# Performance work log

Measured on AMD Instinct MI355X. Metric: run time of the kernel, lower is better.

The kernel has to match this reference:

```python
import jax, jax.numpy as jnp
import numpy as np

B, N, C = 8, 1024, 768
HEADS = 8
HD = C // HEADS  # head_dim = qk_dim // num_heads since qk_ratio=1
SCALE = HD ** (-0.5)


def setup_inputs() -> dict:
    key = jax.random.key(0)
    ks = jax.random.split(key, 8)
    s = 0.02
    return {
        "x": jax.random.normal(ks[0], (B, N, C), dtype=jnp.float32),
        "y": jax.random.normal(ks[1], (B, N, C), dtype=jnp.float32),
        "relative_pos": jax.random.normal(ks[2], (HEADS, N, N), dtype=jnp.float32),
        "H": 32,
        "W": 32,
        "Wq": jax.random.normal(ks[3], (C, C), dtype=jnp.float32) * s,
        "Wk": jax.random.normal(ks[4], (C, C), dtype=jnp.float32) * s,
        "Wv": jax.random.normal(ks[5], (C, C), dtype=jnp.float32) * s,
        "Wp": jax.random.normal(ks[6], (C, C), dtype=jnp.float32) * s,
        "bp": jnp.zeros((C,), dtype=jnp.float32),
    }


def reference(x, y, relative_pos, H, W, Wq, Wk, Wv, Wp, bp):
    # sr_ratio == 1 path: K/V come directly from y (no spatial reduction).
    b, n, c = x.shape
    q = (x @ Wq.T).reshape(b, n, HEADS, HD)       # bnhd
    k = (y @ Wk.T).reshape(b, n, HEADS, HD)       # bmhd
    v = (y @ Wv.T).reshape(b, n, HEADS, HD)       # bmhd
    # scores: QK^T * scale + learned relative position bias (broadcast over batch)
    attn = jnp.einsum("bnhd,bmhd->bhnm", q, k) * SCALE + relative_pos[None]
    attn = jax.nn.softmax(attn, axis=-1)
    out = jnp.einsum("bhnm,bmhd->bnhd", attn, v).reshape(b, n, c)
    return out @ Wp.T + bp
```

## Files before the change

kernel.cpp:

```cpp
#include <hip/hip_runtime.h>
#include <hip/hip_bf16.h>
#include <cstdint>
#include <cstddef>


using f32x4  = __attribute__((ext_vector_type(4))) float;
using bf16x8 = __attribute__((ext_vector_type(8))) __bf16;

constexpr int Bb = 8, Nn = 1024, Cc = 768;
constexpr float LOG2E = 1.4426950408889634f;
constexpr float QSC   = 0.10206207261596575f * 1.4426950408889634f;

__device__ __forceinline__ uint16_t f2bf(float f) {
  union { float f; uint32_t u; } v; v.f = f;
  return (uint16_t)((v.u + 0x7fffu + ((v.u >> 16) & 1u)) >> 16);
}

__device__ __forceinline__ void gl_lds16(const void* g, void* l) {
  __builtin_amdgcn_global_load_lds(
      (const __attribute__((address_space(1))) void*)g,
      (__attribute__((address_space(3))) void*)l, 16, 0, 0);
}

__device__ __forceinline__ f32x4 mfma16(bf16x8 a, bf16x8 b, f32x4 c) {
  return __builtin_amdgcn_mfma_f32_16x16x32_bf16(a, b, c, 0, 0, 0);
}

template <int CTRL>
__device__ __forceinline__ float dpp_add(float v) {
  union { float f; int i; } u, r;
  u.f = v;
  r.i = __builtin_amdgcn_update_dpp(u.i, u.i, CTRL, 0xF, 0xF, false);
  return v + r.f;
}
__device__ __forceinline__ float red16_add(float v) {
  v = dpp_add<0x128>(v);
  v = dpp_add<0x124>(v);
  v = dpp_add<0x122>(v);
  v = dpp_add<0x121>(v);
  return v;
}

__global__ void cvt2_kernel(const float* __restrict__ a,
                            const float* __restrict__ b,
                            uint16_t* __restrict__ da,
                            uint16_t* __restrict__ db, int n4) {
  int i = blockIdx.x * blockDim.x + threadIdx.x;
  const float* s = blockIdx.y ? b : a;
  uint16_t* d = blockIdx.y ? db : da;
  if (i < n4) {
    float4 v = ((const float4*)s)[i];
    ushort4 o;
    o.x = f2bf(v.x); o.y = f2bf(v.y); o.z = f2bf(v.z); o.w = f2bf(v.w);
    ((ushort4*)d)[i] = o;
  }
}

__global__ void cvtw_kernel(const float* __restrict__ wq,
                            const float* __restrict__ wk,
                            const float* __restrict__ wv,
                            const float* __restrict__ wp,
                            uint16_t* __restrict__ dq, uint16_t* __restrict__ dk,
                            uint16_t* __restrict__ dv, uint16_t* __restrict__ dp,
                            int n4) {
  int i = blockIdx.x * blockDim.x + threadIdx.x;
  const float* s; uint16_t* d; float sc = 1.f;
  switch (blockIdx.y) {
    case 0:  s = wq; d = dq; sc = QSC; break;
    case 1:  s = wk; d = dk; break;
    case 2:  s = wv; d = dv; break;
    default: s = wp; d = dp; break;
  }
  if (i < n4) {
    float4 v = ((const float4*)s)[i];
    ushort4 o;
    o.x = f2bf(v.x * sc); o.y = f2bf(v.y * sc);
    o.z = f2bf(v.z * sc); o.w = f2bf(v.w * sc);
    ((ushort4*)d)[i] = o;
  }
}

__device__ __forceinline__ void gemm_core(const uint16_t* __restrict__ A,
                                          const uint16_t* __restrict__ Bt,
                                          int m0, int n0, f32x4 (&acc)[4][4]) {
  __shared__ uint16_t As[128 * 64];
  __shared__ uint16_t Bs[128 * 64];
  const int tid = threadIdx.x;
  const int lane = tid & 63, l16 = lane & 15, quad = lane >> 4;
  const int w = tid >> 6;
  const int wm = (w & 1) * 64, wn = (w >> 1) * 64;

  int soff[4];
#pragma unroll
  for (int i = 0; i < 4; ++i) {
    int idx = tid + 256 * i;
    int row = idx >> 3, pc = idx & 7;
    int c = pc ^ (row & 7);
    soff[i] = row * 768 + c * 8;
  }

  for (int k0 = 0; k0 < 768; k0 += 64) {
    __syncthreads();
#pragma unroll
    for (int i = 0; i < 4; ++i)
      gl_lds16(A + (size_t)m0 * 768 + k0 + soff[i], &As[(tid + 256 * i) * 8]);
#pragma unroll
    for (int i = 0; i < 4; ++i)
      gl_lds16(Bt + (size_t)n0 * 768 + k0 + soff[i], &Bs[(tid + 256 * i) * 8]);
    __syncthreads();

#pragma unroll
    for (int ks = 0; ks < 2; ++ks) {
      bf16x8 a[4], b[4];
      const int phys = (ks * 4 + quad) ^ (l16 & 7);
#pragma unroll
      for (int i = 0; i < 4; ++i)
        a[i] = *(const bf16x8*)&As[(wm + i * 16 + l16) * 64 + phys * 8];
#pragma unroll
      for (int j = 0; j < 4; ++j)
        b[j] = *(const bf16x8*)&Bs[(wn + j * 16 + l16) * 64 + phys * 8];
#pragma unroll
      for (int i = 0; i < 4; ++i)
#pragma unroll
        for (int j = 0; j < 4; ++j)
          acc[i][j] = mfma16(a[i], b[j], acc[i][j]);
    }
  }
}

__global__ __launch_bounds__(256, 3) void qkv_kernel(
    const uint16_t* __restrict__ xb, const uint16_t* __restrict__ yb,
    const uint16_t* __restrict__ wq, const uint16_t* __restrict__ wk,
    const uint16_t* __restrict__ wv, uint16_t* __restrict__ Qb,
    uint16_t* __restrict__ Kb, uint16_t* __restrict__ Vt) {
  const int seg = blockIdx.x / 6, nb = blockIdx.x % 6;
  const uint16_t* A  = (seg == 0) ? xb : yb;
  const uint16_t* Bt = (seg == 0) ? wq : (seg == 1) ? wk : wv;
  const int m0 = blockIdx.y * 128, n0 = nb * 128;

  f32x4 acc[4][4] = {};
  gemm_core(A, Bt, m0, n0, acc);

  const int tid = threadIdx.x, lane = tid & 63;
  const int l16 = lane & 15, quad = lane >> 4, w = tid >> 6;
  const int wm = (w & 1) * 64, wn = (w >> 1) * 64;

  if (seg <= 1) {
    uint16_t* O = seg ? Kb : Qb;
#pragma unroll
    for (int i = 0; i < 4; ++i)
#pragma unroll
      for (int j = 0; j < 4; ++j) {
        int col = n0 + wn + j * 16 + l16;
#pragma unroll
        for (int r = 0; r < 4; ++r) {
          int row = m0 + wm + i * 16 + quad * 4 + r;
          O[(size_t)row * 768 + col] = f2bf(acc[i][j][r]);
        }
      }
  } else {
#pragma unroll
    for (int i = 0; i < 4; ++i) {
      int row0 = m0 + wm + i * 16 + quad * 4;
      int bidx = row0 >> 10, nseq = row0 & 1023;
#pragma unroll
      for (int j = 0; j < 4; ++j) {
        int col = n0 + wn + j * 16 + l16;
        int h = col / 96, hd = col % 96;
        ushort4 pk;
        pk.x = f2bf(acc[i][j][0]); pk.y = f2bf(acc[i][j][1]);
        pk.z = f2bf(acc[i][j][2]); pk.w = f2bf(acc[i][j][3]);
        size_t o = (((size_t)(bidx * 8 + h) * 96 + hd) << 10) + nseq;
        *(ushort4*)(Vt + o) = pk;
      }
    }
  }
}

__global__ __launch_bounds__(256, 3) void proj_kernel(
    const uint16_t* __restrict__ A, const uint16_t* __restrict__ Bt,
    float* __restrict__ out, const float* __restrict__ bias) {
  const int m0 = blockIdx.y * 128, n0 = blockIdx.x * 128;
  f32x4 acc[4][4] = {};
  gemm_core(A, Bt, m0, n0, acc);

  const int tid = threadIdx.x, lane = tid & 63;
  const int l16 = lane & 15, quad = lane >> 4, w = tid >> 6;
  const int wm = (w & 1) * 64, wn = (w >> 1) * 64;
  float bv[4];
#pragma unroll
  for (int j = 0; j < 4; ++j) bv[j] = bias[n0 + wn + j * 16 + l16];
#pragma unroll
  for (int i = 0; i < 4; ++i)
#pragma unroll
    for (int j = 0; j < 4; ++j) {
      int col = n0 + wn + j * 16 + l16;
#pragma unroll
      for (int r = 0; r < 4; ++r) {
        int row = m0 + wm + i * 16 + quad * 4 + r;
        out[(size_t)row * 768 + col] = acc[i][j][r] + bv[j];
      }
    }
}

__global__ __launch_bounds__(512, 4) void attn_kernel(
    const uint16_t* __restrict__ Q,
    const uint16_t* __restrict__ Kb,
    const uint16_t* __restrict__ Vt,
    const float* __restrict__ rel,
    uint16_t* __restrict__ AO) {
  __shared__ uint16_t Ks[2][64 * 96];
  __shared__ uint16_t Vs[2][96 * 64];
  __shared__ uint16_t Ps[128 * 64];

  const int tid = threadIdx.x;
  const int q0 = blockIdx.x * 128;
  const int bh = blockIdx.y;
  const int b = bh >> 3, h = bh & 7;
  const int w = tid >> 6, lane = tid & 63;
  const int l16 = lane & 15, quad = lane >> 4;
  const int l7 = l16 & 7;

  const int qrow = q0 + w * 16 + l16;
  bf16x8 qf[3];
  {
    const uint16_t* qp =
        Q + ((size_t)(b * 1024 + qrow)) * 768 + h * 96 + quad * 8;
#pragma unroll
    for (int j = 0; j < 3; ++j) qf[j] = *(const bf16x8*)(qp + j * 32);
  }

  auto kSrc = [](int c) {
    int r = c / 12, pc = c % 12;
    int kc = (pc < 8) ? (pc ^ (r & 7)) : (8 + ((pc & 3) ^ (r & 3)));
    return r * 768 + kc * 8;
  };
  auto vSrc = [](int c) {
    int d = c >> 3, pc = c & 7;
    return d * 1024 + (pc ^ (d & 7)) * 8;
  };
  const int  kc0 = tid;
  const int  ks0 = kSrc(kc0);
  const bool isK1 = (tid < 256);
  const int  c1 = isK1 ? (512 + tid) : (tid - 256);
  const int  s1 = isK1 ? kSrc(c1) : vSrc(c1);
  const int  vc2 = 256 + tid;
  const int  vs2 = vSrc(vc2);

  const uint16_t* kslab = Kb + ((size_t)(b * 1024)) * 768 + h * 96;
  const uint16_t* vslab = Vt + ((size_t)(bh * 96) << 10);
  const float* relbase =
      rel + ((size_t)h << 20) + ((size_t)(q0 + w * 16 + quad * 4) << 10) + l16;

  auto stage = [&](int knext, int bufi) {
    const uint16_t* kb = kslab + (size_t)knext * 768;
    const uint16_t* vb = vslab + knext;
    uint16_t* Kbuf = &Ks[bufi][0];
    uint16_t* Vbuf = &Vs[bufi][0];
    gl_lds16(kb + ks0, Kbuf + kc0 * 8);
    if (isK1) gl_lds16(kb + s1, Kbuf + c1 * 8);
    else      gl_lds16(vb + s1, Vbuf + c1 * 8);
    gl_lds16(vb + vs2, Vbuf + vc2 * 8);
  };

  float relv[2][16];
  auto loadrel = [&](int knext, float (&dst)[16]) {
#pragma unroll
    for (int r = 0; r < 4; ++r)
#pragma unroll
      for (int nt = 0; nt < 4; ++nt)
        dst[nt * 4 + r] = relbase[(size_t)r * 1024 + knext + nt * 16];
  };

  float l_i[4] = {0.f, 0.f, 0.f, 0.f};
  f32x4 o_acc[6] = {};

  stage(0, 0);
  loadrel(0, relv[0]);

#pragma unroll 2
  for (int kt = 0; kt < 16; ++kt) {
    const int cur = kt & 1, nxt = (kt + 1) & 1;
    __syncthreads();
    if (kt < 15) {
      stage((kt + 1) * 64, nxt);
      loadrel((kt + 1) * 64, relv[nxt]);
    }
    const uint16_t* KsC = &Ks[cur][0];
    const uint16_t* VsC = &Vs[cur][0];
    const float* rv = relv[cur];

    f32x4 s[4] = {};
#pragma unroll
    for (int ksi = 0; ksi < 3; ++ksi) {
#pragma unroll
      for (int nt = 0; nt < 4; ++nt) {
        const int row = nt * 16 + l16;
        const int c = ksi * 4 + quad;
        const int phys =
            (ksi < 2) ? (c ^ (row & 7)) : (8 + ((c & 3) ^ (row & 3)));
        bf16x8 kf = *(const bf16x8*)&KsC[row * 96 + phys * 8];
        s[nt] = mfma16(qf[ksi], kf, s[nt]);
      }
    }

    float pv[16];
#pragma unroll
    for (int nt = 0; nt < 4; ++nt)
#pragma unroll
      for (int r = 0; r < 4; ++r)
        pv[nt * 4 + r] =
            __builtin_amdgcn_exp2f(fmaf(rv[nt * 4 + r], LOG2E, s[nt][r]));
#pragma unroll
    for (int r = 0; r < 4; ++r)
      l_i[r] += (pv[r] + pv[4 + r]) + (pv[8 + r] + pv[12 + r]);

    const int khi = l16 >> 3;
#pragma unroll
    for (int r = 0; r < 4; ++r) {
      const int qloc = quad * 4 + r;
      const int rowoff = (w * 16 + qloc) * 64;
      const int sw = qloc & 7;
#pragma unroll
      for (int nt = 0; nt < 4; ++nt) {
        const int kc = 2 * nt + khi;
        Ps[rowoff + (((kc ^ sw) << 3) | l7)] = f2bf(pv[nt * 4 + r]);
      }
    }
    asm volatile("s_waitcnt lgkmcnt(0)" ::: "memory");

#pragma unroll
    for (int ksi = 0; ksi < 2; ++ksi) {
      const int phys = (ksi * 4 + quad) ^ l7;
      bf16x8 pf = *(const bf16x8*)&Ps[(w * 16 + l16) * 64 + phys * 8];
#pragma unroll
      for (int jt = 0; jt < 6; ++jt) {
        const int d = jt * 16 + l16;
        bf16x8 vf = *(const bf16x8*)&VsC[d * 64 + phys * 8];
        o_acc[jt] = mfma16(pf, vf, o_acc[jt]);
      }
    }
  }

#pragma unroll
  for (int r = 0; r < 4; ++r) {
    float inv = 1.f / red16_add(l_i[r]);
    int row = q0 + w * 16 + quad * 4 + r;
#pragma unroll
    for (int jt = 0; jt < 6; ++jt) {
      int col = h * 96 + jt * 16 + l16;
      AO[(size_t)(b * 1024 + row) * 768 + col] = f2bf(o_acc[jt][r] * inv);
    }
  }
}

extern "C" void kernel_launch(void* const* d_in, const int* in_sizes, int n_in,
                              void* d_out, int out_size, void* d_ws,
                              size_t ws_size, hipStream_t stream) {
  const float* x   = (const float*)d_in[0];
  const float* y   = (const float*)d_in[1];
  const float* rel = (const float*)d_in[2];
  const float* Wq  = (const float*)d_in[5];
  const float* Wk  = (const float*)d_in[6];
  const float* Wv  = (const float*)d_in[7];
  const float* Wp  = (const float*)d_in[8];
  const float* bp  = (const float*)d_in[9];
  float* out = (float*)d_out;

  const size_t nBNC = (size_t)Bb * Nn * Cc;
  const size_t nW = (size_t)Cc * Cc;

  char* ws = (char*)d_ws;
  size_t off = 0;
  auto alloc = [&](size_t bytes) {
    char* p = ws + off;
    off += (bytes + 255) & ~(size_t)255;
    return p;
  };
  uint16_t* xb  = (uint16_t*)alloc(nBNC * 2);
  uint16_t* yb  = (uint16_t*)alloc(nBNC * 2);
  uint16_t* wqb = (uint16_t*)alloc(nW * 2);
  uint16_t* wkb = (uint16_t*)alloc(nW * 2);
  uint16_t* wvb = (uint16_t*)alloc(nW * 2);
  uint16_t* wpb = (uint16_t*)alloc(nW * 2);
  uint16_t* Qb  = (uint16_t*)alloc(nBNC * 2);
  uint16_t* Kb  = (uint16_t*)alloc(nBNC * 2);
  uint16_t* Vtb = (uint16_t*)alloc(nBNC * 2);
  uint16_t* AOb = (uint16_t*)alloc(nBNC * 2);

  cvt2_kernel<<<dim3((int)(nBNC / 4 / 256), 2), 256, 0, stream>>>(
      x, y, xb, yb, (int)(nBNC / 4));
  cvtw_kernel<<<dim3((int)(nW / 4 / 256), 4), 256, 0, stream>>>(
      Wq, Wk, Wv, Wp, wqb, wkb, wvb, wpb, (int)(nW / 4));

  qkv_kernel<<<dim3(18, 64), 256, 0, stream>>>(xb, yb, wqb, wkb, wvb, Qb, Kb,
                                               Vtb);

  attn_kernel<<<dim3(8, 64), 512, 0, stream>>>(Qb, Kb, Vtb, rel, AOb);

  proj_kernel<<<dim3(6, 64), 256, 0, stream>>>(AOb, wpb, out, bp);
}
```

Baseline: 273.0 us.

## Double-buffer GEMM K-loop and halve attention block threads with two query strips per wave

The shared GEMM core now double-buffers its A/B LDS tiles and issues the next k-tile's global-to-LDS loads before computing the current one, removing one barrier per iteration so load latency can overlap with MFMA work. The attention kernel drops from 512 to 256 threads per block, with each wave handling two 16-row query strips. Each K/V fragment read from LDS is therefore reused for twice as many MFMAs, and staging is simplified to three K and three V loads per thread. In exchange, register and LDS pressure rise (launch bounds lowered to 2) and fewer waves are available to hide latency.

Measured after the change: 351.4 us. 1.29x slower.

```diff
diff --git a/kernel.cpp b/kernel.cpp
--- a/kernel.cpp
+++ b/kernel.cpp
@@ -83,8 +83,8 @@
 __device__ __forceinline__ void gemm_core(const uint16_t* __restrict__ A,
                                           const uint16_t* __restrict__ Bt,
                                           int m0, int n0, f32x4 (&acc)[4][4]) {
-  __shared__ uint16_t As[128 * 64];
-  __shared__ uint16_t Bs[128 * 64];
+  __shared__ uint16_t As[2][128 * 64];
+  __shared__ uint16_t Bs[2][128 * 64];
   const int tid = threadIdx.x;
   const int lane = tid & 63, l16 = lane & 15, quad = lane >> 4;
   const int w = tid >> 6;
@@ -99,15 +99,24 @@
     soff[i] = row * 768 + c * 8;
   }
 
-  for (int k0 = 0; k0 < 768; k0 += 64) {
+  const uint16_t* Abase = A + (size_t)m0 * 768;
+  const uint16_t* Bbase = Bt + (size_t)n0 * 768;
+  auto stage = [&](int k0, int buf) {
+#pragma unroll
+    for (int i = 0; i < 4; ++i)
+      gl_lds16(Abase + k0 + soff[i], &As[buf][(tid + 256 * i) * 8]);
+#pragma unroll
+    for (int i = 0; i < 4; ++i)
+      gl_lds16(Bbase + k0 + soff[i], &Bs[buf][(tid + 256 * i) * 8]);
+  };
+
+  stage(0, 0);
+
+#pragma unroll 2
+  for (int kt = 0; kt < 12; ++kt) {
+    const int cur = kt & 1, nxt = (kt + 1) & 1;
     __syncthreads();
-#pragma unroll
-    for (int i = 0; i < 4; ++i)
-      gl_lds16(A + (size_t)m0 * 768 + k0 + soff[i], &As[(tid + 256 * i) * 8]);
-#pragma unroll
-    for (int i = 0; i < 4; ++i)
-      gl_lds16(Bt + (size_t)n0 * 768 + k0 + soff[i], &Bs[(tid + 256 * i) * 8]);
-    __syncthreads();
+    if (kt < 11) stage((kt + 1) * 64, nxt);
 
 #pragma unroll
     for (int ks = 0; ks < 2; ++ks) {
@@ -115,10 +124,10 @@
       const int phys = (ks * 4 + quad) ^ (l16 & 7);
 #pragma unroll
       for (int i = 0; i < 4; ++i)
-        a[i] = *(const bf16x8*)&As[(wm + i * 16 + l16) * 64 + phys * 8];
+        a[i] = *(const bf16x8*)&As[cur][(wm + i * 16 + l16) * 64 + phys * 8];
 #pragma unroll
       for (int j = 0; j < 4; ++j)
-        b[j] = *(const bf16x8*)&Bs[(wn + j * 16 + l16) * 64 + phys * 8];
+        b[j] = *(const bf16x8*)&Bs[cur][(wn + j * 16 + l16) * 64 + phys * 8];
 #pragma unroll
       for (int i = 0; i < 4; ++i)
 #pragma unroll
@@ -128,7 +137,7 @@
   }
 }
 
-__global__ __launch_bounds__(256, 3) void qkv_kernel(
+__global__ __launch_bounds__(256, 2) void qkv_kernel(
     const uint16_t* __restrict__ xb, const uint16_t* __restrict__ yb,
     const uint16_t* __restrict__ wq, const uint16_t* __restrict__ wk,
     const uint16_t* __restrict__ wv, uint16_t* __restrict__ Qb,
@@ -177,7 +186,7 @@
   }
 }
 
-__global__ __launch_bounds__(256, 3) void proj_kernel(
+__global__ __launch_bounds__(256, 2) void proj_kernel(
     const uint16_t* __restrict__ A, const uint16_t* __restrict__ Bt,
     float* __restrict__ out, const float* __restrict__ bias) {
   const int m0 = blockIdx.y * 128, n0 = blockIdx.x * 128;
@@ -203,7 +212,7 @@
     }
 }
 
-__global__ __launch_bounds__(512, 4) void attn_kernel(
+__global__ __launch_bounds__(256, 2) void attn_kernel(
     const uint16_t* __restrict__ Q,
     const uint16_t* __restrict__ Kb,
     const uint16_t* __restrict__ Vt,
@@ -221,13 +230,14 @@
   const int l16 = lane & 15, quad = lane >> 4;
   const int l7 = l16 & 7;
 
-  const int qrow = q0 + w * 16 + l16;
-  bf16x8 qf[3];
-  {
+  bf16x8 qf[2][3];
+#pragma unroll
+  for (int st = 0; st < 2; ++st) {
+    const int qrow = q0 + st * 64 + w * 16 + l16;
     const uint16_t* qp =
         Q + ((size_t)(b * 1024 + qrow)) * 768 + h * 96 + quad * 8;
 #pragma unroll
-    for (int j = 0; j < 3; ++j) qf[j] = *(const bf16x8*)(qp + j * 32);
+    for (int j = 0; j < 3; ++j) qf[st][j] = *(const bf16x8*)(qp + j * 32);
   }
 
   auto kSrc = [](int c) {
@@ -239,41 +249,44 @@
     int d = c >> 3, pc = c & 7;
     return d * 1024 + (pc ^ (d & 7)) * 8;
   };
-  const int  kc0 = tid;
-  const int  ks0 = kSrc(kc0);
-  const bool isK1 = (tid < 256);
-  const int  c1 = isK1 ? (512 + tid) : (tid - 256);
-  const int  s1 = isK1 ? kSrc(c1) : vSrc(c1);
-  const int  vc2 = 256 + tid;
-  const int  vs2 = vSrc(vc2);
+  int koffs[3], voffs[3];
+#pragma unroll
+  for (int i = 0; i < 3; ++i) {
+    koffs[i] = kSrc(tid + 256 * i);
+    voffs[i] = vSrc(tid + 256 * i);
+  }
 
   const uint16_t* kslab = Kb + ((size_t)(b * 1024)) * 768 + h * 96;
   const uint16_t* vslab = Vt + ((size_t)(bh * 96) << 10);
-  const float* relbase =
+  const float* relbase0 =
       rel + ((size_t)h << 20) + ((size_t)(q0 + w * 16 + quad * 4) << 10) + l16;
+  const float* relbase1 = relbase0 + (64 << 10);
 
   auto stage = [&](int knext, int bufi) {
     const uint16_t* kb = kslab + (size_t)knext * 768;
     const uint16_t* vb = vslab + knext;
     uint16_t* Kbuf = &Ks[bufi][0];
     uint16_t* Vbuf = &Vs[bufi][0];
-    gl_lds16(kb + ks0, Kbuf + kc0 * 8);
-    if (isK1) gl_lds16(kb + s1, Kbuf + c1 * 8);
-    else      gl_lds16(vb + s1, Vbuf + c1 * 8);
-    gl_lds16(vb + vs2, Vbuf + vc2 * 8);
-  };
-
-  float relv[2][16];
-  auto loadrel = [&](int knext, float (&dst)[16]) {
+#pragma unroll
+    for (int i = 0; i < 3; ++i) {
+      gl_lds16(kb + koffs[i], Kbuf + (tid + 256 * i) * 8);
+      gl_lds16(vb + voffs[i], Vbuf + (tid + 256 * i) * 8);
+    }
+  };
+
+  float relv[2][2][16];
+  auto loadrel = [&](int knext, float (&dst)[2][16]) {
 #pragma unroll
     for (int r = 0; r < 4; ++r)
 #pragma unroll
-      for (int nt = 0; nt < 4; ++nt)
-        dst[nt * 4 + r] = relbase[(size_t)r * 1024 + knext + nt * 16];
-  };
-
-  float l_i[4] = {0.f, 0.f, 0.f, 0.f};
-  f32x4 o_acc[6] = {};
+      for (int nt = 0; nt < 4; ++nt) {
+        dst[0][nt * 4 + r] = relbase0[(size_t)r * 1024 + knext + nt * 16];
+        dst[1][nt * 4 + r] = relbase1[(size_t)r * 1024 + knext + nt * 16];
+      }
+  };
+
+  float l_i[2][4] = {};
+  f32x4 o_acc[2][6] = {};
 
   stage(0, 0);
   loadrel(0, relv[0]);
@@ -288,9 +301,8 @@
     }
     const uint16_t* KsC = &Ks[cur][0];
     const uint16_t* VsC = &Vs[cur][0];
-    const float* rv = relv[cur];
-
-    f32x4 s[4] = {};
+
+    f32x4 s[2][4] = {};
 #pragma unroll
     for (int ksi = 0; ksi < 3; ++ksi) {
 #pragma unroll
@@ -300,31 +312,34 @@
         const int phys =
             (ksi < 2) ? (c ^ (row & 7)) : (8 + ((c & 3) ^ (row & 3)));
         bf16x8 kf = *(const bf16x8*)&KsC[row * 96 + phys * 8];
-        s[nt] = mfma16(qf[ksi], kf, s[nt]);
-      }
-    }
-
-    float pv[16];
-#pragma unroll
-    for (int nt = 0; nt < 4; ++nt)
+        s[0][nt] = mfma16(qf[0][ksi], kf, s[0][nt]);
+        s[1][nt] = mfma16(qf[1][ksi], kf, s[1][nt]);
+      }
+    }
+
+    const int khi = l16 >> 3;
+#pragma unroll
+    for (int st = 0; st < 2; ++st) {
+      float pv[16];
+#pragma unroll
+      for (int nt = 0; nt < 4; ++nt)
+#pragma unroll
+        for (int r = 0; r < 4; ++r)
+          pv[nt * 4 + r] = __builtin_amdgcn_exp2f(
+              fmaf(relv[cur][st][nt * 4 + r], LOG2E, s[st][nt][r]));
 #pragma unroll
       for (int r = 0; r < 4; ++r)
-        pv[nt * 4 + r] =
-            __builtin_amdgcn_exp2f(fmaf(rv[nt * 4 + r], LOG2E, s[nt][r]));
-#pragma unroll
-    for (int r = 0; r < 4; ++r)
-      l_i[r] += (pv[r] + pv[4 + r]) + (pv[8 + r] + pv[12 + r]);
-
-    const int khi = l16 >> 3;
-#pragma unroll
-    for (int r = 0; r < 4; ++r) {
-      const int qloc = quad * 4 + r;
-      const int rowoff = (w * 16 + qloc) * 64;
-      const int sw = qloc & 7;
-#pragma unroll
-      for (int nt = 0; nt < 4; ++nt) {
-        const int kc = 2 * nt + khi;
-        Ps[rowoff + (((kc ^ sw) << 3) | l7)] = f2bf(pv[nt * 4 + r]);
+        l_i[st][r] += (pv[r] + pv[4 + r]) + (pv[8 + r] + pv[12 + r]);
+#pragma unroll
+      for (int r = 0; r < 4; ++r) {
+        const int qloc = quad * 4 + r;
+        const int rowoff = (st * 64 + w * 16 + qloc) * 64;
+        const int sw = qloc & 7;
+#pragma unroll
+        for (int nt = 0; nt < 4; ++nt) {
+          const int kc = 2 * nt + khi;
+          Ps[rowoff + (((kc ^ sw) << 3) | l7)] = f2bf(pv[nt * 4 + r]);
+        }
       }
     }
     asm volatile("s_waitcnt lgkmcnt(0)" ::: "memory");
@@ -332,26 +347,30 @@
 #pragma unroll
     for (int ksi = 0; ksi < 2; ++ksi) {
       const int phys = (ksi * 4 + quad) ^ l7;
-      bf16x8 pf = *(const bf16x8*)&Ps[(w * 16 + l16) * 64 + phys * 8];
+      bf16x8 pf0 = *(const bf16x8*)&Ps[(w * 16 + l16) * 64 + phys * 8];
+      bf16x8 pf1 = *(const bf16x8*)&Ps[(64 + w * 16 + l16) * 64 + phys * 8];
 #pragma unroll
       for (int jt = 0; jt < 6; ++jt) {
         const int d = jt * 16 + l16;
         bf16x8 vf = *(const bf16x8*)&VsC[d * 64 + phys * 8];
-        o_acc[jt] = mfma16(pf, vf, o_acc[jt]);
-      }
-    }
-  }
-
-#pragma unroll
-  for (int r = 0; r < 4; ++r) {
-    float inv = 1.f / red16_add(l_i[r]);
-    int row = q0 + w * 16 + quad * 4 + r;
-#pragma unroll
-    for (int jt = 0; jt < 6; ++jt) {
-      int col = h * 96 + jt * 16 + l16;
-      AO[(size_t)(b * 1024 + row) * 768 + col] = f2bf(o_acc[jt][r] * inv);
-    }
-  }
+        o_acc[0][jt] = mfma16(pf0, vf, o_acc[0][jt]);
+        o_acc[1][jt] = mfma16(pf1, vf, o_acc[1][jt]);
+      }
+    }
+  }
+
+#pragma unroll
+  for (int st = 0; st < 2; ++st)
+#pragma unroll
+    for (int r = 0; r < 4; ++r) {
+      float inv = 1.f / red16_add(l_i[st][r]);
+      int row = q0 + st * 64 + w * 16 + quad * 4 + r;
+#pragma unroll
+      for (int jt = 0; jt < 6; ++jt) {
+        int col = h * 96 + jt * 16 + l16;
+        AO[(size_t)(b * 1024 + row) * 768 + col] = f2bf(o_acc[st][jt][r] * inv);
+      }
+    }
 }
 
 extern "C" void kernel_launch(void* const* d_in, const int* in_sizes, int n_in,
@@ -396,7 +415,7 @@
   qkv_kernel<<<dim3(18, 64), 256, 0, stream>>>(xb, yb, wqb, wkb, wvb, Qb, Kb,
                                                Vtb);
 
-  attn_kernel<<<dim3(8, 64), 512, 0, stream>>>(Qb, Kb, Vtb, rel, AOb);
+  attn_kernel<<<dim3(8, 64), 256, 0, stream>>>(Qb, Kb, Vtb, rel, AOb);
 
   proj_kernel<<<dim3(6, 64), 256, 0, stream>>>(AOb, wpb, out, bp);
 }
```
